# Performance work log

Hardware: AMD Instinct MI355X
Metric: run time of the kernel (lower is better)

The kernel has to match this reference:

```python
import jax, jax.numpy as jnp
import numpy as np

# Trellis-walk LUT dequantization (QTIP-style), reference for QuantizedLinear.materialize()
M, N = 8192, 8192          # payload['shape']
TX, TY, V, L_BITS = 16, 16, 2, 16
T_STEPS = TX * TY // V     # walk length per tile = 128
NUM_TILES = (M // TX) * (N // TY)  # 262144
W_SCALE = 0.011            # payload['W_scale']


def setup_inputs() -> dict:
    key = jax.random.key(0)
    k1, k2, k3, k4 = jax.random.split(key, 4)
    # precomputed trellis walk states: indices into the 2^L-entry LUT
    walks = jax.random.randint(k1, (NUM_TILES, T_STEPS), 0, 2 ** L_BITS, dtype=jnp.int64)
    # trainable LUT: 2^L states, each decoding to V float values
    lut = jax.random.normal(k2, (2 ** L_BITS, V), dtype=jnp.float32)
    # per-row / per-column sign flips (+-1)
    sign_l = jnp.where(jax.random.normal(k3, (M,)) >= 0, 1.0, -1.0).astype(jnp.float32)
    sign_r = jnp.where(jax.random.normal(k4, (N,)) >= 0, 1.0, -1.0).astype(jnp.float32)
    return {"walks": walks, "lut": lut, "sign_l": sign_l, "sign_r": sign_r}


def reference(walks, lut, sign_l, sign_r):
    # Gather V values per walk step: (num_tiles, T, V)
    vals = lut[walks]
    # Reassemble tiles into the dense weight. Tiles are laid out row-major
    # over the (M//Tx, N//Ty) tile grid; each tile is Tx x Ty.
    tiles = vals.reshape(M // TX, N // TY, TX, TY)
    W = tiles.transpose(0, 2, 1, 3).reshape(M, N)
    # per-element sign flips (rank-1 sign pattern) and global scale
    return (W_SCALE * sign_l)[:, None] * W * sign_r[None, :]
```

## Files before the change

### kernel.cpp

```cpp
#include <hip/hip_runtime.h>
#include <hip/hip_bf16.h>

__global__ __launch_bounds__(256) void trellis_dequant(
    const int* __restrict__ walks,
    const float* __restrict__ lut,
    const float* __restrict__ sign_l,
    const float* __restrict__ sign_r,
    float* __restrict__ out)
{
    const int tid = blockIdx.x * 256 + threadIdx.x;
    const int r  = tid >> 9;
    const int tc = tid & 511;
    const int i  = r & 15;
    const int tr = r >> 4;
    const size_t t = (size_t)tr * 512 + (size_t)tc;

    const int4* wp = (const int4*)(walks + t * 128 + i * 8);
    const int4 a = wp[0];
    const int4 b = wp[1];

    const float2* lut2 = (const float2*)lut;
    const float2 v0 = lut2[a.x];
    const float2 v1 = lut2[a.y];
    const float2 v2 = lut2[a.z];
    const float2 v3 = lut2[a.w];
    const float2 v4 = lut2[b.x];
    const float2 v5 = lut2[b.y];
    const float2 v6 = lut2[b.z];
    const float2 v7 = lut2[b.w];

    const float sl = 0.011f * sign_l[r];
    const float4* srp = (const float4*)(sign_r + tc * 16);
    const float4 s0 = srp[0];
    const float4 s1 = srp[1];
    const float4 s2 = srp[2];
    const float4 s3 = srp[3];

    float4 o0, o1, o2, o3;
    o0.x = v0.x * (sl * s0.x);
    o0.y = v0.y * (sl * s0.y);
    o0.z = v1.x * (sl * s0.z);
    o0.w = v1.y * (sl * s0.w);
    o1.x = v2.x * (sl * s1.x);
    o1.y = v2.y * (sl * s1.y);
    o1.z = v3.x * (sl * s1.z);
    o1.w = v3.y * (sl * s1.w);
    o2.x = v4.x * (sl * s2.x);
    o2.y = v4.y * (sl * s2.y);
    o2.z = v5.x * (sl * s2.z);
    o2.w = v5.y * (sl * s2.w);
    o3.x = v6.x * (sl * s3.x);
    o3.y = v6.y * (sl * s3.y);
    o3.z = v7.x * (sl * s3.z);
    o3.w = v7.y * (sl * s3.w);

    float4* op = (float4*)(out + (size_t)r * 8192 + (size_t)tc * 16);
    op[0] = o0;
    op[1] = o1;
    op[2] = o2;
    op[3] = o3;
}

extern "C" void kernel_launch(void* const* d_in, const int* in_sizes, int n_in,
                              void* d_out, int out_size, void* d_ws, size_t ws_size,
                              hipStream_t stream) {
    const int*   walks  = (const int*)d_in[0];
    const float* lut    = (const float*)d_in[1];
    const float* sign_l = (const float*)d_in[2];
    const float* sign_r = (const float*)d_in[3];
    float* out = (float*)d_out;

    trellis_dequant<<<16384, 256, 0, stream>>>(walks, lut, sign_l, sign_r, out);
}
```

Before: 492.0 us.

## Stage walk indices through LDS and coalesce output stores per block

Each block now loads 16 contiguous tiles of walk indices into shared memory using coalesced nontemporal vector loads, then remaps threads so each wavefront writes contiguous float4 segments of an output row. This replaces the old per-thread strided 32-byte walk reads and the 64-byte-per-thread output writes that were scattered across rows. Stores are marked nontemporal to avoid cache pollution. The cost is an LDS round trip and a barrier per block.

```diff
diff --git a/kernel.cpp b/kernel.cpp
--- a/kernel.cpp
+++ b/kernel.cpp
@@ -1,5 +1,8 @@
 #include <hip/hip_runtime.h>
-#include <hip/hip_bf16.h>
+
+
+typedef int   int4v   __attribute__((ext_vector_type(4)));
+typedef float float4v __attribute__((ext_vector_type(4)));
 
 __global__ __launch_bounds__(256) void trellis_dequant(
     const int* __restrict__ walks,
@@ -8,57 +11,48 @@
     const float* __restrict__ sign_r,
     float* __restrict__ out)
 {
-    const int tid = blockIdx.x * 256 + threadIdx.x;
-    const int r  = tid >> 9;
-    const int tc = tid & 511;
-    const int i  = r & 15;
-    const int tr = r >> 4;
-    const size_t t = (size_t)tr * 512 + (size_t)tc;
+    __shared__ int4v wlds4[512];
 
-    const int4* wp = (const int4*)(walks + t * 128 + i * 8);
-    const int4 a = wp[0];
-    const int4 b = wp[1];
+    const int b   = blockIdx.x;
+    const int T0  = b << 4;
+    const int tr  = T0 >> 9;
+    const int tc0 = T0 & 511;
 
-    const float2* lut2 = (const float2*)lut;
-    const float2 v0 = lut2[a.x];
-    const float2 v1 = lut2[a.y];
-    const float2 v2 = lut2[a.z];
-    const float2 v3 = lut2[a.w];
-    const float2 v4 = lut2[b.x];
-    const float2 v5 = lut2[b.y];
-    const float2 v6 = lut2[b.z];
-    const float2 v7 = lut2[b.w];
+    const int4v* gw = (const int4v*)(walks + (size_t)T0 * 128);
+    const int t = threadIdx.x;
+    wlds4[t]       = __builtin_nontemporal_load(gw + t);
+    wlds4[t + 256] = __builtin_nontemporal_load(gw + t + 256);
+    __syncthreads();
+
+    const int2*   wlds2 = (const int2*)wlds4;
+    const float2* lut2  = (const float2*)lut;
+
+    const int l = threadIdx.x & 63;
+    const int w = threadIdx.x >> 6;
+    const int i = (w << 2) + (l >> 4);
+    const int r = (tr << 4) + i;
 
     const float sl = 0.011f * sign_l[r];
-    const float4* srp = (const float4*)(sign_r + tc * 16);
-    const float4 s0 = srp[0];
-    const float4 s1 = srp[1];
-    const float4 s2 = srp[2];
-    const float4 s3 = srp[3];
+    const float4* srp = (const float4*)sign_r + (size_t)tc0 * 4;
+    float4v* op = (float4v*)(out + (size_t)r * 8192 + (size_t)tc0 * 16);
 
-    float4 o0, o1, o2, o3;
-    o0.x = v0.x * (sl * s0.x);
-    o0.y = v0.y * (sl * s0.y);
-    o0.z = v1.x * (sl * s0.z);
-    o0.w = v1.y * (sl * s0.w);
-    o1.x = v2.x * (sl * s1.x);
-    o1.y = v2.y * (sl * s1.y);
-    o1.z = v3.x * (sl * s1.z);
-    o1.w = v3.y * (sl * s1.w);
-    o2.x = v4.x * (sl * s2.x);
-    o2.y = v4.y * (sl * s2.y);
-    o2.z = v5.x * (sl * s2.z);
-    o2.w = v5.y * (sl * s2.w);
-    o3.x = v6.x * (sl * s3.x);
-    o3.y = v6.y * (sl * s3.y);
-    o3.z = v7.x * (sl * s3.z);
-    o3.w = v7.y * (sl * s3.w);
-
-    float4* op = (float4*)(out + (size_t)r * 8192 + (size_t)tc * 16);
-    op[0] = o0;
-    op[1] = o1;
-    op[2] = o2;
-    op[3] = o3;
+    const int base_f = l & 15;
+#pragma unroll
+    for (int s = 0; s < 4; ++s) {
+        const int f = base_f + (s << 4);
+        const int j = f >> 2;
+        const int q = f & 3;
+        const int2 wpair = wlds2[j * 64 + i * 4 + q];
+        const float2 v0 = lut2[wpair.x];
+        const float2 v1 = lut2[wpair.y];
+        const float4 sr = srp[f];
+        float4v o;
+        o.x = v0.x * (sl * sr.x);
+        o.y = v0.y * (sl * sr.y);
+        o.z = v1.x * (sl * sr.z);
+        o.w = v1.y * (sl * sr.w);
+        __builtin_nontemporal_store(o, op + f);
+    }
 }
 
 extern "C" void kernel_launch(void* const* d_in, const int* in_sizes, int n_in,
```

Measured after the change: 431.2 us. 12.3% less time.
